# Optimization experiments

Hardware: AMD Instinct MI355X
Metric: run time of the kernel (lower is better)

Reference implementation:

```python
import jax, jax.numpy as jnp
import numpy as np

SPLINE_ORDER = 3


def _bspline_basis(x, knots, k, order):
    """Cox-de Boor recursion with static (python float) knots, matching the torch code exactly."""
    if order == 0:
        if k + 1 >= len(knots):
            return jnp.zeros_like(x)
        return ((knots[k] <= x) & (x < knots[k + 1])).astype(x.dtype)
    left = 0.0
    right = 0.0
    if k + order < len(knots) and knots[k + order] != knots[k]:
        left = (x - knots[k]) / (knots[k + order] - knots[k]) * _bspline_basis(x, knots, k, order - 1)
    if k + order + 1 < len(knots) and knots[k + order + 1] != knots[k + 1]:
        right = (knots[k + order + 1] - x) / (knots[k + order + 1] - knots[k + 1]) * _bspline_basis(x, knots, k + 1, order - 1)
    return left + right


def setup_inputs() -> dict:
    key = jax.random.key(0)
    k1, k2, k3 = jax.random.split(key, 3)
    B, S, IN, OUT, NUM_KNOTS = 16, 4096, 256, 256, 5
    x = jax.random.normal(k1, (B, S, IN), dtype=jnp.float32)
    inner_coeffs = jax.random.normal(k2, (IN, NUM_KNOTS), dtype=jnp.float32) * 0.1
    outer_coeffs = jax.random.normal(k3, (OUT, IN), dtype=jnp.float32) * 0.1
    return {"x": x, "inner_coeffs": inner_coeffs, "outer_coeffs": outer_coeffs}


def reference(x, inner_coeffs, outer_coeffs):
    in_dim, num_knots = inner_coeffs.shape
    # knots = linspace(-1, 1, num_knots + spline_order), static python floats
    knots = np.linspace(-1.0, 1.0, num_knots + SPLINE_ORDER).tolist()
    xt = jnp.tanh(x)  # [B, S, I]
    # Original loops k in range(num_knots - spline_order); remaining basis columns stay zero,
    # so only the first n_active inner coefficients contribute.
    n_active = num_knots - SPLINE_ORDER
    basis = jnp.stack(
        [_bspline_basis(xt, knots, k, SPLINE_ORDER) for k in range(n_active)], axis=-1
    )  # [B, S, I, n_active]
    inner = jnp.einsum('bsik,ik->bsi', basis, inner_coeffs[:, :n_active])  # [B, S, I]
    return jnp.einsum('bsi,oi->bso', inner, outer_coeffs)  # [B, S, O]
```

## Files before the change

### kernel.cpp

```cpp
#include <hip/hip_runtime.h>
#include <hip/hip_bf16.h>
#include <stdint.h>


typedef __attribute__((ext_vector_type(8))) short short8;
typedef __attribute__((ext_vector_type(16))) float f32x16;

__device__ __forceinline__ uint16_t f2bf(float f) {
    union { float f; uint32_t u; } v; v.f = f;
    uint32_t r = v.u + 0x7FFFu + ((v.u >> 16) & 1u);
    return (uint16_t)(r >> 16);
}

__device__ __forceinline__ uint32_t pack_bf2(float lo, float hi) {
    __hip_bfloat162 h = __float22bfloat162_rn(make_float2(lo, hi));
    union { __hip_bfloat162 h; uint32_t u; } v; v.h = h;
    return v.u;
}

__device__ __forceinline__ float cube_relu(float v) {
    float m = fmaxf(v, 0.0f);
    return m * m * m;
}

__device__ __forceinline__ float inner_eval(float xx, float c0, float c1) {
    float e  = __expf(2.0f * xx);
    float t  = 1.0f - 2.0f * __builtin_amdgcn_rcpf(e + 1.0f);
    float u  = (t + 1.0f) * 3.5f;
    float w0 = cube_relu(u);
    float w1 = cube_relu(u - 1.0f);
    float w2 = cube_relu(u - 2.0f);
    float w3 = cube_relu(u - 3.0f);
    float w4 = cube_relu(u - 4.0f);
    float w5 = cube_relu(u - 5.0f);
    float B0 = w0 - 4.0f*w1 + 6.0f*w2 - 4.0f*w3 + w4;
    float B1 = w1 - 4.0f*w2 + 6.0f*w3 - 4.0f*w4 + w5;
    return (c0 * B0 + c1 * B1) * (1.0f / 6.0f);
}

__device__ __forceinline__ void load_lds16(const void* g, void* l) {
    __builtin_amdgcn_global_load_lds(
        (const __attribute__((address_space(1))) uint32_t*)g,
        (__attribute__((address_space(3))) uint32_t*)l, 16, 0, 0);
}

__global__ void conv_w(const float4* __restrict__ wf, char* __restrict__ o) {
    const int i = blockIdx.x * blockDim.x + threadIdx.x;
    const float4 v = wf[i];
    uint2 r;
    r.x = (uint32_t)f2bf(v.x) | ((uint32_t)f2bf(v.y) << 16);
    r.y = (uint32_t)f2bf(v.z) | ((uint32_t)f2bf(v.w) << 16);
    const int row = i >> 6;
    const int cb  = (i & 63) << 3;
    *(uint2*)(o + row * 512 + (cb ^ ((row & 7) << 4))) = r;
}

__global__ void __launch_bounds__(512, 2) kan_fused(const float* __restrict__ x,
                                                    const float* __restrict__ ic,
                                                    const char* __restrict__ wb,
                                                    float* __restrict__ out)
{
    __shared__ __align__(16) char smem[133120];
    char*   Wlds = smem;
    float2* C2   = (float2*)(smem + 131072);

    const int t    = threadIdx.x;
    const int lane = t & 63;
    const int w    = t >> 6;
    const int col  = lane & 31;
    const int half = lane >> 5;
    const int swz  = (col & 7) << 4;

    const int mb = blockIdx.x * 256 + w * 32;
    const float* xp = x + (size_t)(mb + col) * 256 + half * 8;

    float4 xa = *(const float4*)(xp);
    float4 xb = *(const float4*)(xp + 4);

    if (t < 256) C2[t] = make_float2(ic[t * 5 + 0], ic[t * 5 + 1]);

    #pragma unroll
    for (int it = 0; it < 16; ++it) {
        const int base = ((it * 8 + w) << 10) + lane * 16;
        load_lds16(wb + base, Wlds + base);
    }
    __syncthreads();

    f32x16 acc[8];
    #pragma unroll
    for (int j = 0; j < 8; ++j)
        #pragma unroll
        for (int r = 0; r < 16; ++r)
            acc[j][r] = 0.0f;

    #pragma unroll 1
    for (int kk = 0; kk < 16; ++kk) {
        const int cw = (kk * 32 + half * 16) ^ swz;
        short8 b[8];
        #pragma unroll
        for (int j = 0; j < 8; ++j)
            b[j] = *(const short8*)(Wlds + ((j * 32 + col) << 9) + cw);

        float4 xa_n = xa, xb_n = xb;
        if (kk < 15) {
            xa_n = *(const float4*)(xp + (kk + 1) * 16);
            xb_n = *(const float4*)(xp + (kk + 1) * 16 + 4);
        }

        const int gk = kk * 16 + half * 8;
        const float4 cA = *(const float4*)(&C2[gk + 0]);
        const float4 cB = *(const float4*)(&C2[gk + 2]);
        const float4 cC = *(const float4*)(&C2[gk + 4]);
        const float4 cD = *(const float4*)(&C2[gk + 6]);

        float v0 = inner_eval(xa.x, cA.x, cA.y);
        float v1 = inner_eval(xa.y, cA.z, cA.w);
        float v2 = inner_eval(xa.z, cB.x, cB.y);
        float v3 = inner_eval(xa.w, cB.z, cB.w);
        float v4 = inner_eval(xb.x, cC.x, cC.y);
        float v5 = inner_eval(xb.y, cC.z, cC.w);
        float v6 = inner_eval(xb.z, cD.x, cD.y);
        float v7 = inner_eval(xb.w, cD.z, cD.w);

        union { short8 v; uint32_t u[4]; } af;
        af.u[0] = pack_bf2(v0, v1);
        af.u[1] = pack_bf2(v2, v3);
        af.u[2] = pack_bf2(v4, v5);
        af.u[3] = pack_bf2(v6, v7);

        #pragma unroll
        for (int j = 0; j < 8; ++j)
            acc[j] = __builtin_amdgcn_mfma_f32_32x32x16_bf16(af.v, b[j], acc[j], 0, 0, 0);

        xa = xa_n; xb = xb_n;
    }

    float* op = out + (size_t)(mb + 4 * half) * 256 + col;
    #pragma unroll
    for (int j = 0; j < 8; ++j) {
        #pragma unroll
        for (int r = 0; r < 16; ++r)
            op[(size_t)((r & 3) + 8 * (r >> 2)) * 256 + j * 32] = acc[j][r];
    }
}

extern "C" void kernel_launch(void* const* d_in, const int* in_sizes, int n_in,
                              void* d_out, int out_size, void* d_ws, size_t ws_size,
                              hipStream_t stream) {
    const float* x  = (const float*)d_in[0];
    const float* ic = (const float*)d_in[1];
    const float* oc = (const float*)d_in[2];
    char* wb = (char*)d_ws;

    conv_w<<<64, 256, 0, stream>>>((const float4*)oc, wb);
    kan_fused<<<256, 512, 0, stream>>>(x, ic, wb, (float*)d_out);
}
```

Baseline: 130.2 us.

## Split spline evaluation into separate kernel staging bf16 activations in output buffer

Splits the fused kernel in two. A new kernel evaluates the tanh and B-spline inner function over all elements and writes bf16 activations, in the MFMA-friendly row layout, into the output buffer. A pure GEMM kernel then reads those activations from the output region it will overwrite and accumulates with the LDS-resident weights, with the k-loop now fully unrolled. The inner coefficients are also packed into the workspace during weight conversion. This removes the transcendental and spline math from the MFMA loop and gives it full-grid parallelism, at the cost of an extra global write and read of the activation matrix, one more launch, and reliance on in-place aliasing between the staged activations and the output.

```diff
diff --git a/kernel.cpp b/kernel.cpp
--- a/kernel.cpp
+++ b/kernel.cpp
@@ -44,7 +44,8 @@
         (__attribute__((address_space(3))) uint32_t*)l, 16, 0, 0);
 }
 
-__global__ void conv_w(const float4* __restrict__ wf, char* __restrict__ o) {
+__global__ void conv_w(const float* __restrict__ ic, const float4* __restrict__ wf,
+                       char* __restrict__ o) {
     const int i = blockIdx.x * blockDim.x + threadIdx.x;
     const float4 v = wf[i];
     uint2 r;
@@ -53,16 +54,44 @@
     const int row = i >> 6;
     const int cb  = (i & 63) << 3;
     *(uint2*)(o + row * 512 + (cb ^ ((row & 7) << 4))) = r;
+    if (i < 256)
+        *(float2*)(o + 131072 + i * 8) = make_float2(ic[i * 5 + 0], ic[i * 5 + 1]);
 }
 
-__global__ void __launch_bounds__(512, 2) kan_fused(const float* __restrict__ x,
-                                                    const float* __restrict__ ic,
-                                                    const char* __restrict__ wb,
-                                                    float* __restrict__ out)
-{
-    __shared__ __align__(16) char smem[133120];
-    char*   Wlds = smem;
-    float2* C2   = (float2*)(smem + 131072);
+__global__ void __launch_bounds__(256) spline_a(const float* __restrict__ x,
+                                                const char* __restrict__ wb,
+                                                char* __restrict__ ab) {
+    const int g  = blockIdx.x * 256 + threadIdx.x;
+    const int m  = g >> 5;
+    const int kb = (g & 31) << 3;
+    const float4 xa = *(const float4*)(x + (size_t)m * 256 + kb);
+    const float4 xb = *(const float4*)(x + (size_t)m * 256 + kb + 4);
+    const float4* c2g = (const float4*)(wb + 131072);
+    const float4 cA = c2g[(kb >> 1) + 0];
+    const float4 cB = c2g[(kb >> 1) + 1];
+    const float4 cC = c2g[(kb >> 1) + 2];
+    const float4 cD = c2g[(kb >> 1) + 3];
+    float v0 = inner_eval(xa.x, cA.x, cA.y);
+    float v1 = inner_eval(xa.y, cA.z, cA.w);
+    float v2 = inner_eval(xa.z, cB.x, cB.y);
+    float v3 = inner_eval(xa.w, cB.z, cB.w);
+    float v4 = inner_eval(xb.x, cC.x, cC.y);
+    float v5 = inner_eval(xb.y, cC.z, cC.w);
+    float v6 = inner_eval(xb.z, cD.x, cD.y);
+    float v7 = inner_eval(xb.w, cD.z, cD.w);
+    uint4 r;
+    r.x = pack_bf2(v0, v1);
+    r.y = pack_bf2(v2, v3);
+    r.z = pack_bf2(v4, v5);
+    r.w = pack_bf2(v6, v7);
+    char* A = ab + ((size_t)(m >> 8) << 18) + (((m >> 5) & 7) << 15)
+                 + ((m & 31) << 9) + (kb << 1);
+    *(uint4*)A = r;
+}
+
+__global__ void __launch_bounds__(512, 2) kan_gemm(const char* __restrict__ wb,
+                                                   float* __restrict__ out) {
+    __shared__ __align__(16) char Wlds[131072];
 
     const int t    = threadIdx.x;
     const int lane = t & 63;
@@ -71,19 +100,15 @@
     const int half = lane >> 5;
     const int swz  = (col & 7) << 4;
 
-    const int mb = blockIdx.x * 256 + w * 32;
-    const float* xp = x + (size_t)(mb + col) * 256 + half * 8;
-
-    float4 xa = *(const float4*)(xp);
-    float4 xb = *(const float4*)(xp + 4);
-
-    if (t < 256) C2[t] = make_float2(ic[t * 5 + 0], ic[t * 5 + 1]);
-
     #pragma unroll
     for (int it = 0; it < 16; ++it) {
         const int base = ((it * 8 + w) << 10) + lane * 16;
         load_lds16(wb + base, Wlds + base);
     }
+
+    const char* Ar = (const char*)out + ((size_t)blockIdx.x << 18)
+                   + (w << 15) + (col << 9) + (half << 4);
+
     __syncthreads();
 
     f32x16 acc[8];
@@ -93,48 +118,20 @@
         for (int r = 0; r < 16; ++r)
             acc[j][r] = 0.0f;
 
-    #pragma unroll 1
+    #pragma unroll
     for (int kk = 0; kk < 16; ++kk) {
+        const short8 av = *(const short8*)(Ar + kk * 32);
         const int cw = (kk * 32 + half * 16) ^ swz;
         short8 b[8];
         #pragma unroll
         for (int j = 0; j < 8; ++j)
             b[j] = *(const short8*)(Wlds + ((j * 32 + col) << 9) + cw);
-
-        float4 xa_n = xa, xb_n = xb;
-        if (kk < 15) {
-            xa_n = *(const float4*)(xp + (kk + 1) * 16);
-            xb_n = *(const float4*)(xp + (kk + 1) * 16 + 4);
-        }
-
-        const int gk = kk * 16 + half * 8;
-        const float4 cA = *(const float4*)(&C2[gk + 0]);
-        const float4 cB = *(const float4*)(&C2[gk + 2]);
-        const float4 cC = *(const float4*)(&C2[gk + 4]);
-        const float4 cD = *(const float4*)(&C2[gk + 6]);
-
-        float v0 = inner_eval(xa.x, cA.x, cA.y);
-        float v1 = inner_eval(xa.y, cA.z, cA.w);
-        float v2 = inner_eval(xa.z, cB.x, cB.y);
-        float v3 = inner_eval(xa.w, cB.z, cB.w);
-        float v4 = inner_eval(xb.x, cC.x, cC.y);
-        float v5 = inner_eval(xb.y, cC.z, cC.w);
-        float v6 = inner_eval(xb.z, cD.x, cD.y);
-        float v7 = inner_eval(xb.w, cD.z, cD.w);
-
-        union { short8 v; uint32_t u[4]; } af;
-        af.u[0] = pack_bf2(v0, v1);
-        af.u[1] = pack_bf2(v2, v3);
-        af.u[2] = pack_bf2(v4, v5);
-        af.u[3] = pack_bf2(v6, v7);
-
         #pragma unroll
         for (int j = 0; j < 8; ++j)
-            acc[j] = __builtin_amdgcn_mfma_f32_32x32x16_bf16(af.v, b[j], acc[j], 0, 0, 0);
-
-        xa = xa_n; xb = xb_n;
+            acc[j] = __builtin_amdgcn_mfma_f32_32x32x16_bf16(av, b[j], acc[j], 0, 0, 0);
     }
 
+    const int mb = blockIdx.x * 256 + w * 32;
     float* op = out + (size_t)(mb + 4 * half) * 256 + col;
     #pragma unroll
     for (int j = 0; j < 8; ++j) {
@@ -152,6 +149,7 @@
     const float* oc = (const float*)d_in[2];
     char* wb = (char*)d_ws;
 
-    conv_w<<<64, 256, 0, stream>>>((const float4*)oc, wb);
-    kan_fused<<<256, 512, 0, stream>>>(x, ic, wb, (float*)d_out);
+    conv_w<<<64, 256, 0, stream>>>(ic, (const float4*)oc, wb);
+    spline_a<<<8192, 256, 0, stream>>>(x, wb, (char*)d_out);
+    kan_gemm<<<256, 512, 0, stream>>>(wb, (float*)d_out);
 }
```

Result: slower. 136.4 us (+4.8%).
